# Kernel tuning notes

Hardware: AMD Instinct MI355X
Metric: run time of the kernel (lower is better)

Reference implementation:

```python
import jax, jax.numpy as jnp
import numpy as np
from jax import lax

B, C, H, W = 16, 128, 128, 128
COUT, KH, KW, K, RED, TEMP = 128, 3, 3, 4, 4, 30.0
ATTN_CH = max(C // RED, 1)

def setup_inputs() -> dict:
    key = jax.random.key(0)
    ks = jax.random.split(key, 7)
    fan_out = COUT * KH * KW
    std = np.sqrt(2.0 / fan_out)  # kaiming_normal fan_out, relu
    return {
        "x": jax.random.normal(ks[0], (B, C, H, W), dtype=jnp.float32),
        "weight": jax.random.normal(ks[1], (K, COUT, C, KH, KW), dtype=jnp.float32) * std,
        "bias": jnp.zeros((K, COUT), dtype=jnp.float32),
        "aw1": jax.random.normal(ks[2], (ATTN_CH, C), dtype=jnp.float32) * (1.0 / np.sqrt(C)),
        "ab1": jnp.zeros((ATTN_CH,), dtype=jnp.float32),
        "aw2": jax.random.normal(ks[3], (K, ATTN_CH), dtype=jnp.float32) * (1.0 / np.sqrt(ATTN_CH)),
        "ab2": jnp.zeros((K,), dtype=jnp.float32),
    }

def reference(x, weight, bias, aw1, ab1, aw2, ab2):
    # Attention branch: global avg pool -> 1x1 conv -> relu -> 1x1 conv
    pooled = jnp.mean(x, axis=(2, 3))                       # (B, C)
    h = jax.nn.relu(pooled @ aw1.T + ab1)                   # (B, attn_ch)
    scores = h @ aw2.T + ab2                                # (B, K)
    attn = jax.nn.softmax(scores / TEMP, axis=1)            # (B, K)

    # Per-sample aggregated kernel and bias
    agg_w = jnp.einsum('bk,koipq->boipq', attn, weight)     # (B, Cout, Cin, kH, kW)
    agg_b = attn @ bias                                     # (B, Cout)

    # Per-sample conv2d (stride 1, padding 1, dilation 1, groups 1)
    def conv_one(xi, wi):
        return lax.conv_general_dilated(
            xi[None], wi,
            window_strides=(1, 1),
            padding=((1, 1), (1, 1)),
            dimension_numbers=('NCHW', 'OIHW', 'NCHW'),
        )[0]

    out = jax.vmap(conv_one)(x, agg_w)                      # (B, Cout, H, W)
    return out + agg_b[:, :, None, None]
```

## Files before the change

kernel.cpp:

```cpp
#include <hip/hip_runtime.h>

typedef float f32x4 __attribute__((ext_vector_type(4)));
typedef short bf16x8 __attribute__((ext_vector_type(8)));

__device__ __forceinline__ unsigned short f2bf(float f) {
  unsigned u = __builtin_bit_cast(unsigned, f);
  u = (u + 0x7FFFu + ((u >> 16) & 1u)) >> 16;
  return (unsigned short)u;
}

__device__ __forceinline__ void async16(const unsigned short* g, unsigned short* l) {
  __builtin_amdgcn_global_load_lds(
      (__attribute__((address_space(1))) void*)g,
      (__attribute__((address_space(3))) void*)l, 16, 0, 0);
}

#define XT_ROW 16640

__global__ __launch_bounds__(256) void k_transpose(const float* __restrict__ x,
                                                   unsigned short* __restrict__ xt,
                                                   float* __restrict__ rowsum) {
  __shared__ unsigned short tile[128][128];
  __shared__ float psum[128][8];
  const int y = blockIdx.x, b = blockIdx.y;
  const int t = threadIdx.x;
  const int colb = (t & 7) * 16;
  const int cp = t >> 3;
  const int swz = (t & 7) << 3;
  for (int ci = 0; ci < 4; ++ci) {
    const int c = ci * 32 + cp;
    const int c2 = c ^ swz;
    const float* src = x + (((size_t)(b * 128 + c) * 128 + y) * 128 + colb);
    float s = 0.f;
#pragma unroll
    for (int j = 0; j < 16; j += 4) {
      float4 v = *(const float4*)(src + j);
      s += v.x + v.y + v.z + v.w;
      tile[colb + j + 0][c2] = f2bf(v.x);
      tile[colb + j + 1][c2] = f2bf(v.y);
      tile[colb + j + 2][c2] = f2bf(v.z);
      tile[colb + j + 3][c2] = f2bf(v.w);
    }
    psum[c][t & 7] = s;
  }
  __syncthreads();
#pragma unroll
  for (int it = 0; it < 8; ++it) {
    const int slot = t + it * 256;
    const int col = slot >> 4;
    const int cg = (slot & 15) * 8;
    const int c2 = cg ^ (((col >> 4) & 7) << 3);
    uint4 vv = *(const uint4*)&tile[col][c2];
    *(uint4*)(xt + (((size_t)b * 130 + y + 1) * 130 + col + 1) * 128 + cg) = vv;
  }
  if (t < 128) {
    float r = 0.f;
#pragma unroll
    for (int j = 0; j < 8; ++j) r += psum[t][j];
    rowsum[((size_t)b * 128 + t) * 128 + y] = r;
  }
}

__global__ __launch_bounds__(256) void k_border(unsigned short* __restrict__ xt) {
  const int b = blockIdx.y;
  const int idx = blockIdx.x * 256 + threadIdx.x;
  if (idx >= 8256) return;
  int row, col, ck;
  if (idx < 4160) {
    row = (idx < 2080) ? 0 : 129;
    const int s = idx % 2080;
    col = s >> 4;
    ck = s & 15;
  } else {
    const int s = idx - 4160;
    row = (s >> 5) + 1;
    col = (s & 16) ? 129 : 0;
    ck = s & 15;
  }
  uint4 z = {0, 0, 0, 0};
  *(uint4*)(xt + ((size_t)b * 130 + row) * 130 * 128 + (size_t)col * 128 + ck * 8) = z;
}

__global__ __launch_bounds__(128) void k_attn(const float* __restrict__ rowsum,
                                              const float* __restrict__ aw1,
                                              const float* __restrict__ ab1,
                                              const float* __restrict__ aw2,
                                              const float* __restrict__ ab2,
                                              const float* __restrict__ bias,
                                              float* __restrict__ attn,
                                              float* __restrict__ aggb) {
  __shared__ float pooled[128];
  __shared__ float h[32];
  __shared__ float at[4];
  const int b = blockIdx.x, t = threadIdx.x;
  const float* rs = rowsum + (size_t)(b * 128 + t) * 128;
  float s = 0.f;
  for (int yy = 0; yy < 128; ++yy) s += rs[yy];
  pooled[t] = s * (1.f / 16384.f);
  __syncthreads();
  if (t < 32) {
    float hv = ab1[t];
    for (int c = 0; c < 128; ++c) hv += pooled[c] * aw1[t * 128 + c];
    h[t] = fmaxf(hv, 0.f);
  }
  __syncthreads();
  if (t < 4) {
    float sc = ab2[t];
    for (int a = 0; a < 32; ++a) sc += h[a] * aw2[t * 32 + a];
    at[t] = sc * (1.f / 30.f);
  }
  __syncthreads();
  if (t == 0) {
    float m = fmaxf(fmaxf(at[0], at[1]), fmaxf(at[2], at[3]));
    float e0 = __expf(at[0] - m), e1 = __expf(at[1] - m);
    float e2 = __expf(at[2] - m), e3 = __expf(at[3] - m);
    float inv = 1.f / (e0 + e1 + e2 + e3);
    at[0] = e0 * inv; at[1] = e1 * inv; at[2] = e2 * inv; at[3] = e3 * inv;
  }
  __syncthreads();
  if (t < 4) attn[b * 4 + t] = at[t];
  float ab = 0.f;
  for (int k = 0; k < 4; ++k) ab += at[k] * bias[k * 128 + t];
  aggb[b * 128 + t] = ab;
}

__global__ __launch_bounds__(256) void k_aggw(const float* __restrict__ weight,
                                              const float* __restrict__ attn,
                                              unsigned short* __restrict__ aggw) {
  const int fid = blockIdx.x * 256 + threadIdx.x;
  const int kk = fid & 63;
  const int o = (fid >> 6) & 127;
  const int rest = fid >> 13;
  const int s = rest % 18;
  const int b = rest / 18;
  const int c = ((s & 1) << 6) + kk;
  const int pq = s >> 1;
  const size_t src = (size_t)o * 1152 + (size_t)c * 9 + pq;
  float v = attn[b * 4 + 0] * weight[src]
          + attn[b * 4 + 1] * weight[src + 147456]
          + attn[b * 4 + 2] * weight[src + 2 * 147456]
          + attn[b * 4 + 3] * weight[src + 3 * 147456];
  aggw[fid] = f2bf(v);
}

__global__ __launch_bounds__(512, 1) void k_conv(const unsigned short* __restrict__ xt,
                                                 const unsigned short* __restrict__ aggw,
                                                 const float* __restrict__ aggb,
                                                 float* __restrict__ out) {
  __shared__ unsigned short lds[73728];
  const int id = blockIdx.x;
  const int swz = (id & 7) * 128 + (id >> 3);
  const int b = swz >> 6;
  const int Y = (swz & 63) * 2;
  const int t = threadIdx.x;
  const int lane = t & 63, w = t >> 6;
  const int mw = w >> 2, nw = w & 3;
  const int l15 = lane & 15, lk = lane >> 4;
  const int e7 = l15 & 7;
  const int sl0 = (lk ^ e7) * 8;
  const int sl1 = ((4 ^ lk) ^ e7) * 8;
  const int baseA0 = (mw * 64 + l15) * 64 + sl0;
  const int baseA1 = (mw * 64 + l15) * 64 + sl1;
  const int baseB0 = 8192 + (nw * 64 + l15) * 64 + sl0;
  const int baseB1 = 8192 + (nw * 64 + l15) * 64 + sl1;

  const unsigned short* aS[2];
#pragma unroll
  for (int i = 0; i < 2; ++i) {
    const int c = i * 512 + t, o = c >> 3, k8 = c & 7;
    aS[i] = aggw + (size_t)b * 147456 + o * 64 + ((k8 ^ (o & 7)) * 8);
  }
  const unsigned short* bS[4];
#pragma unroll
  for (int i = 0; i < 4; ++i) {
    const int c = i * 512 + t, n = c >> 3, k8 = c & 7;
    const int r = n >> 7, col = n & 127;
    bS[i] = xt + ((size_t)(b * 130 + Y + r) * 130 + col) * 128 + ((k8 ^ (n & 7)) * 8);
  }

#define STA(jw, s2, i) async16(aS[i] + (s2) * 8192,                            \
                               &lds[(jw) * 24576 + ((i) * 512 + w * 64) * 8])
#define STB(jw, i, p2, q2, c02) async16(bS[i] + (p2) * XT_ROW + (q2) * 128 + (c02), \
                               &lds[(jw) * 24576 + 8192 + ((i) * 512 + w * 64) * 8])

  STA(0, 0, 0); STA(0, 0, 1);
  STB(0, 0, 0, 0, 0); STB(0, 1, 0, 0, 0); STB(0, 2, 0, 0, 0); STB(0, 3, 0, 0, 0);
  STA(1, 1, 0); STA(1, 1, 1);
  STB(1, 0, 0, 0, 64); STB(1, 1, 0, 0, 64); STB(1, 2, 0, 0, 64); STB(1, 3, 0, 0, 64);

  f32x4 acc[4][4] = {};

#pragma unroll
  for (int s = 0; s < 18; ++s) {
    const int jb = (s % 3) * 24576;
    const int s2 = s + 2, jw = s2 % 3;
    const int tap2 = s2 >> 1;
    const int p2 = tap2 / 3, q2 = tap2 - 3 * p2, c02 = (s2 & 1) << 6;
    const bool st = (s2 < 18);

    if (s < 17) { asm volatile("s_waitcnt vmcnt(6)" ::: "memory"); }
    else        { asm volatile("s_waitcnt vmcnt(0)" ::: "memory"); }
    __builtin_amdgcn_sched_barrier(0);
    __builtin_amdgcn_s_barrier();
    __builtin_amdgcn_sched_barrier(0);

    bf16x8 a0, a1, a2, a3, b0, b1, b2, b3;
    b0 = *(const bf16x8*)(&lds[jb + baseB0 + 0 * 1024]);
    b1 = *(const bf16x8*)(&lds[jb + baseB0 + 1 * 1024]);
    b2 = *(const bf16x8*)(&lds[jb + baseB0 + 2 * 1024]);
    b3 = *(const bf16x8*)(&lds[jb + baseB0 + 3 * 1024]);
    a0 = *(const bf16x8*)(&lds[jb + baseA0 + 0 * 1024]);
    a1 = *(const bf16x8*)(&lds[jb + baseA0 + 1 * 1024]);
    if (st) { STA(jw, s2, 0); STA(jw, s2, 1); }
    __builtin_amdgcn_s_barrier();
    __builtin_amdgcn_s_setprio(1);
    acc[0][0] = __builtin_amdgcn_mfma_f32_16x16x32_bf16(a0, b0, acc[0][0], 0, 0, 0);
    acc[0][1] = __builtin_amdgcn_mfma_f32_16x16x32_bf16(a0, b1, acc[0][1], 0, 0, 0);
    acc[0][2] = __builtin_amdgcn_mfma_f32_16x16x32_bf16(a0, b2, acc[0][2], 0, 0, 0);
    acc[0][3] = __builtin_amdgcn_mfma_f32_16x16x32_bf16(a0, b3, acc[0][3], 0, 0, 0);
    acc[1][0] = __builtin_amdgcn_mfma_f32_16x16x32_bf16(a1, b0, acc[1][0], 0, 0, 0);
    acc[1][1] = __builtin_amdgcn_mfma_f32_16x16x32_bf16(a1, b1, acc[1][1], 0, 0, 0);
    acc[1][2] = __builtin_amdgcn_mfma_f32_16x16x32_bf16(a1, b2, acc[1][2], 0, 0, 0);
    acc[1][3] = __builtin_amdgcn_mfma_f32_16x16x32_bf16(a1, b3, acc[1][3], 0, 0, 0);
    __builtin_amdgcn_s_setprio(0);
    __builtin_amdgcn_s_barrier();
    a2 = *(const bf16x8*)(&lds[jb + baseA0 + 2 * 1024]);
    a3 = *(const bf16x8*)(&lds[jb + baseA0 + 3 * 1024]);
    if (st) { STB(jw, 0, p2, q2, c02); STB(jw, 1, p2, q2, c02); }
    __builtin_amdgcn_s_barrier();
    __builtin_amdgcn_s_setprio(1);
    acc[2][0] = __builtin_amdgcn_mfma_f32_16x16x32_bf16(a2, b0, acc[2][0], 0, 0, 0);
    acc[2][1] = __builtin_amdgcn_mfma_f32_16x16x32_bf16(a2, b1, acc[2][1], 0, 0, 0);
    acc[2][2] = __builtin_amdgcn_mfma_f32_16x16x32_bf16(a2, b2, acc[2][2], 0, 0, 0);
    acc[2][3] = __builtin_amdgcn_mfma_f32_16x16x32_bf16(a2, b3, acc[2][3], 0, 0, 0);
    acc[3][0] = __builtin_amdgcn_mfma_f32_16x16x32_bf16(a3, b0, acc[3][0], 0, 0, 0);
    acc[3][1] = __builtin_amdgcn_mfma_f32_16x16x32_bf16(a3, b1, acc[3][1], 0, 0, 0);
    acc[3][2] = __builtin_amdgcn_mfma_f32_16x16x32_bf16(a3, b2, acc[3][2], 0, 0, 0);
    acc[3][3] = __builtin_amdgcn_mfma_f32_16x16x32_bf16(a3, b3, acc[3][3], 0, 0, 0);
    __builtin_amdgcn_s_setprio(0);
    __builtin_amdgcn_s_barrier();
    b0 = *(const bf16x8*)(&lds[jb + baseB1 + 0 * 1024]);
    b1 = *(const bf16x8*)(&lds[jb + baseB1 + 1 * 1024]);
    b2 = *(const bf16x8*)(&lds[jb + baseB1 + 2 * 1024]);
    b3 = *(const bf16x8*)(&lds[jb + baseB1 + 3 * 1024]);
    a0 = *(const bf16x8*)(&lds[jb + baseA1 + 0 * 1024]);
    a1 = *(const bf16x8*)(&lds[jb + baseA1 + 1 * 1024]);
    if (st) { STB(jw, 2, p2, q2, c02); STB(jw, 3, p2, q2, c02); }
    __builtin_amdgcn_s_barrier();
    __builtin_amdgcn_s_setprio(1);
    acc[0][0] = __builtin_amdgcn_mfma_f32_16x16x32_bf16(a0, b0, acc[0][0], 0, 0, 0);
    acc[0][1] = __builtin_amdgcn_mfma_f32_16x16x32_bf16(a0, b1, acc[0][1], 0, 0, 0);
    acc[0][2] = __builtin_amdgcn_mfma_f32_16x16x32_bf16(a0, b2, acc[0][2], 0, 0, 0);
    acc[0][3] = __builtin_amdgcn_mfma_f32_16x16x32_bf16(a0, b3, acc[0][3], 0, 0, 0);
    acc[1][0] = __builtin_amdgcn_mfma_f32_16x16x32_bf16(a1, b0, acc[1][0], 0, 0, 0);
    acc[1][1] = __builtin_amdgcn_mfma_f32_16x16x32_bf16(a1, b1, acc[1][1], 0, 0, 0);
    acc[1][2] = __builtin_amdgcn_mfma_f32_16x16x32_bf16(a1, b2, acc[1][2], 0, 0, 0);
    acc[1][3] = __builtin_amdgcn_mfma_f32_16x16x32_bf16(a1, b3, acc[1][3], 0, 0, 0);
    __builtin_amdgcn_s_setprio(0);
    __builtin_amdgcn_s_barrier();
    a2 = *(const bf16x8*)(&lds[jb + baseA1 + 2 * 1024]);
    a3 = *(const bf16x8*)(&lds[jb + baseA1 + 3 * 1024]);
    __builtin_amdgcn_s_barrier();
    __builtin_amdgcn_s_setprio(1);
    acc[2][0] = __builtin_amdgcn_mfma_f32_16x16x32_bf16(a2, b0, acc[2][0], 0, 0, 0);
    acc[2][1] = __builtin_amdgcn_mfma_f32_16x16x32_bf16(a2, b1, acc[2][1], 0, 0, 0);
    acc[2][2] = __builtin_amdgcn_mfma_f32_16x16x32_bf16(a2, b2, acc[2][2], 0, 0, 0);
    acc[2][3] = __builtin_amdgcn_mfma_f32_16x16x32_bf16(a2, b3, acc[2][3], 0, 0, 0);
    acc[3][0] = __builtin_amdgcn_mfma_f32_16x16x32_bf16(a3, b0, acc[3][0], 0, 0, 0);
    acc[3][1] = __builtin_amdgcn_mfma_f32_16x16x32_bf16(a3, b1, acc[3][1], 0, 0, 0);
    acc[3][2] = __builtin_amdgcn_mfma_f32_16x16x32_bf16(a3, b2, acc[3][2], 0, 0, 0);
    acc[3][3] = __builtin_amdgcn_mfma_f32_16x16x32_bf16(a3, b3, acc[3][3], 0, 0, 0);
    __builtin_amdgcn_s_setprio(0);
  }
#undef STA
#undef STB

  const int y = Y + (nw >> 1);
  const int colb = (nw & 1) * 64 + l15;
#pragma unroll
  for (int mi = 0; mi < 4; ++mi) {
    const int o = mw * 64 + mi * 16 + lk * 4;
#pragma unroll
    for (int rr = 0; rr < 4; ++rr) {
      const float bsv = aggb[b * 128 + o + rr];
      float* orow = out + ((size_t)(b * 128 + o + rr) * 128 + y) * 128 + colb;
      orow[0]  = acc[mi][0][rr] + bsv;
      orow[16] = acc[mi][1][rr] + bsv;
      orow[32] = acc[mi][2][rr] + bsv;
      orow[48] = acc[mi][3][rr] + bsv;
    }
  }
}

extern "C" void kernel_launch(void* const* d_in, const int* in_sizes, int n_in,
                              void* d_out, int out_size, void* d_ws, size_t ws_size,
                              hipStream_t stream) {
  const float* x      = (const float*)d_in[0];
  const float* weight = (const float*)d_in[1];
  const float* bias   = (const float*)d_in[2];
  const float* aw1    = (const float*)d_in[3];
  const float* ab1    = (const float*)d_in[4];
  const float* aw2    = (const float*)d_in[5];
  const float* ab2    = (const float*)d_in[6];
  float* out = (float*)d_out;

  char* ws = (char*)d_ws;
  unsigned short* xt   = (unsigned short*)ws;
  unsigned short* aggw = (unsigned short*)(ws + 69222400);
  float* rowsum        = (float*)(ws + 69222400 + 4718592);
  float* attn          = (float*)(ws + 69222400 + 4718592 + 1048576);
  float* aggb          = (float*)(ws + 69222400 + 4718592 + 1048576 + 256);

  hipLaunchKernelGGL(k_border, dim3(33, 16), dim3(256), 0, stream, xt);
  hipLaunchKernelGGL(k_transpose, dim3(128, 16), dim3(256), 0, stream, x, xt, rowsum);
  hipLaunchKernelGGL(k_attn, dim3(16), dim3(128), 0, stream,
                     rowsum, aw1, ab1, aw2, ab2, bias, attn, aggb);
  hipLaunchKernelGGL(k_aggw, dim3(9216), dim3(256), 0, stream, weight, attn, aggw);
  hipLaunchKernelGGL(k_conv, dim3(1024), dim3(512), 0, stream, xt, aggw, aggb, out);
}
```

Measured before the change: 157.8 us.

## Enlarge conv tile to four rows per block with double-buffered LDS

The conv kernel now computes a full 128-output-channel by 4-row (512-pixel) tile per block, with each wave owning all 128 output channels and 64 pixels. The grid is halved and each weight chunk is reused across twice as many pixels. The three-stage LDS ring with prefetch distance two is replaced by a two-buffer scheme with a full vmcnt(0) wait each step, and launch bounds now ask for two blocks per CU. Accumulators per thread double, raising register pressure, and the shallower prefetch may expose load latency.

```diff
diff --git a/kernel.cpp b/kernel.cpp
--- a/kernel.cpp
+++ b/kernel.cpp
@@ -143,26 +143,26 @@
   aggw[fid] = f2bf(v);
 }
 
-__global__ __launch_bounds__(512, 1) void k_conv(const unsigned short* __restrict__ xt,
+__global__ __launch_bounds__(512, 2) void k_conv(const unsigned short* __restrict__ xt,
                                                  const unsigned short* __restrict__ aggw,
                                                  const float* __restrict__ aggb,
                                                  float* __restrict__ out) {
-  __shared__ unsigned short lds[73728];
+  __shared__ unsigned short lds[81920];
   const int id = blockIdx.x;
-  const int swz = (id & 7) * 128 + (id >> 3);
-  const int b = swz >> 6;
-  const int Y = (swz & 63) * 2;
+  const int swz = (id & 7) * 64 + (id >> 3);
+  const int b = swz >> 5;
+  const int Y = (swz & 31) * 4;
   const int t = threadIdx.x;
-  const int lane = t & 63, w = t >> 6;
-  const int mw = w >> 2, nw = w & 3;
+  const int lane = t & 63, nw = t >> 6;
   const int l15 = lane & 15, lk = lane >> 4;
   const int e7 = l15 & 7;
   const int sl0 = (lk ^ e7) * 8;
   const int sl1 = ((4 ^ lk) ^ e7) * 8;
-  const int baseA0 = (mw * 64 + l15) * 64 + sl0;
-  const int baseA1 = (mw * 64 + l15) * 64 + sl1;
-  const int baseB0 = 8192 + (nw * 64 + l15) * 64 + sl0;
-  const int baseB1 = 8192 + (nw * 64 + l15) * 64 + sl1;
+  const int baseA0 = l15 * 64 + sl0;
+  const int baseA1 = l15 * 64 + sl1;
+  const int nrow = (nw >> 1) * 128 + (nw & 1) * 64 + l15;
+  const int baseB0 = 8192 + nrow * 64 + sl0;
+  const int baseB1 = 8192 + nrow * 64 + sl1;
 
   const unsigned short* aS[2];
 #pragma unroll
@@ -170,36 +170,37 @@
     const int c = i * 512 + t, o = c >> 3, k8 = c & 7;
     aS[i] = aggw + (size_t)b * 147456 + o * 64 + ((k8 ^ (o & 7)) * 8);
   }
-  const unsigned short* bS[4];
-#pragma unroll
-  for (int i = 0; i < 4; ++i) {
+  const unsigned short* bS[8];
+#pragma unroll
+  for (int i = 0; i < 8; ++i) {
     const int c = i * 512 + t, n = c >> 3, k8 = c & 7;
     const int r = n >> 7, col = n & 127;
-    bS[i] = xt + ((size_t)(b * 130 + Y + r) * 130 + col) * 128 + ((k8 ^ (n & 7)) * 8);
-  }
-
-#define STA(jw, s2, i) async16(aS[i] + (s2) * 8192,                            \
-                               &lds[(jw) * 24576 + ((i) * 512 + w * 64) * 8])
-#define STB(jw, i, p2, q2, c02) async16(bS[i] + (p2) * XT_ROW + (q2) * 128 + (c02), \
-                               &lds[(jw) * 24576 + 8192 + ((i) * 512 + w * 64) * 8])
+    bS[i] = xt + ((size_t)(b * 130 + Y + r) * 130 + col) * 128 + ((k8 ^ (col & 7)) * 8);
+  }
+
+  const int wu = (t >> 6) * 64;
+#define STA(jb, sv, i) async16(aS[i] + (size_t)(sv) * 8192,                    \
+                               &lds[(jb) + ((i) * 512 + wu) * 8])
+#define STB(jb, pqv, i) async16(bS[i] + (pqv),                                 \
+                               &lds[(jb) + 8192 + ((i) * 512 + wu) * 8])
 
   STA(0, 0, 0); STA(0, 0, 1);
-  STB(0, 0, 0, 0, 0); STB(0, 1, 0, 0, 0); STB(0, 2, 0, 0, 0); STB(0, 3, 0, 0, 0);
-  STA(1, 1, 0); STA(1, 1, 1);
-  STB(1, 0, 0, 0, 64); STB(1, 1, 0, 0, 64); STB(1, 2, 0, 0, 64); STB(1, 3, 0, 0, 64);
-
-  f32x4 acc[4][4] = {};
+#pragma unroll
+  for (int i = 0; i < 8; ++i) STB(0, 0, i);
+
+  f32x4 acc[8][4] = {};
 
 #pragma unroll
   for (int s = 0; s < 18; ++s) {
-    const int jb = (s % 3) * 24576;
-    const int s2 = s + 2, jw = s2 % 3;
-    const int tap2 = s2 >> 1;
-    const int p2 = tap2 / 3, q2 = tap2 - 3 * p2, c02 = (s2 & 1) << 6;
-    const bool st = (s2 < 18);
-
-    if (s < 17) { asm volatile("s_waitcnt vmcnt(6)" ::: "memory"); }
-    else        { asm volatile("s_waitcnt vmcnt(0)" ::: "memory"); }
+    const int jb = (s & 1) * 40960;
+    const int jn = ((s + 1) & 1) * 40960;
+    const int s1 = s + 1;
+    const int tap1 = s1 >> 1;
+    const int p1 = tap1 / 3, q1 = tap1 - 3 * p1;
+    const int pq1 = (p1 * 130 + q1) * 128 + ((s1 & 1) << 6);
+    const bool st = (s1 < 18);
+
+    asm volatile("s_waitcnt vmcnt(0)" ::: "memory");
     __builtin_amdgcn_sched_barrier(0);
     __builtin_amdgcn_s_barrier();
     __builtin_amdgcn_sched_barrier(0);
@@ -211,32 +212,40 @@
     b3 = *(const bf16x8*)(&lds[jb + baseB0 + 3 * 1024]);
     a0 = *(const bf16x8*)(&lds[jb + baseA0 + 0 * 1024]);
     a1 = *(const bf16x8*)(&lds[jb + baseA0 + 1 * 1024]);
-    if (st) { STA(jw, s2, 0); STA(jw, s2, 1); }
-    __builtin_amdgcn_s_barrier();
-    __builtin_amdgcn_s_setprio(1);
-    acc[0][0] = __builtin_amdgcn_mfma_f32_16x16x32_bf16(a0, b0, acc[0][0], 0, 0, 0);
-    acc[0][1] = __builtin_amdgcn_mfma_f32_16x16x32_bf16(a0, b1, acc[0][1], 0, 0, 0);
-    acc[0][2] = __builtin_amdgcn_mfma_f32_16x16x32_bf16(a0, b2, acc[0][2], 0, 0, 0);
-    acc[0][3] = __builtin_amdgcn_mfma_f32_16x16x32_bf16(a0, b3, acc[0][3], 0, 0, 0);
-    acc[1][0] = __builtin_amdgcn_mfma_f32_16x16x32_bf16(a1, b0, acc[1][0], 0, 0, 0);
-    acc[1][1] = __builtin_amdgcn_mfma_f32_16x16x32_bf16(a1, b1, acc[1][1], 0, 0, 0);
-    acc[1][2] = __builtin_amdgcn_mfma_f32_16x16x32_bf16(a1, b2, acc[1][2], 0, 0, 0);
-    acc[1][3] = __builtin_amdgcn_mfma_f32_16x16x32_bf16(a1, b3, acc[1][3], 0, 0, 0);
-    __builtin_amdgcn_s_setprio(0);
-    __builtin_amdgcn_s_barrier();
     a2 = *(const bf16x8*)(&lds[jb + baseA0 + 2 * 1024]);
     a3 = *(const bf16x8*)(&lds[jb + baseA0 + 3 * 1024]);
-    if (st) { STB(jw, 0, p2, q2, c02); STB(jw, 1, p2, q2, c02); }
-    __builtin_amdgcn_s_barrier();
+    if (st) { STA(jn, s1, 0); STA(jn, s1, 1); STB(jn, pq1, 0); STB(jn, pq1, 1); }
+    __builtin_amdgcn_sched_barrier(0);
+    __builtin_amdgcn_s_barrier();
+    __builtin_amdgcn_sched_barrier(0);
     __builtin_amdgcn_s_setprio(1);
-    acc[2][0] = __builtin_amdgcn_mfma_f32_16x16x32_bf16(a2, b0, acc[2][0], 0, 0, 0);
-    acc[2][1] = __builtin_amdgcn_mfma_f32_16x16x32_bf16(a2, b1, acc[2][1], 0, 0, 0);
-    acc[2][2] = __builtin_amdgcn_mfma_f32_16x16x32_bf16(a2, b2, acc[2][2], 0, 0, 0);
-    acc[2][3] = __builtin_amdgcn_mfma_f32_16x16x32_bf16(a2, b3, acc[2][3], 0, 0, 0);
-    acc[3][0] = __builtin_amdgcn_mfma_f32_16x16x32_bf16(a3, b0, acc[3][0], 0, 0, 0);
-    acc[3][1] = __builtin_amdgcn_mfma_f32_16x16x32_bf16(a3, b1, acc[3][1], 0, 0, 0);
-    acc[3][2] = __builtin_amdgcn_mfma_f32_16x16x32_bf16(a3, b2, acc[3][2], 0, 0, 0);
-    acc[3][3] = __builtin_amdgcn_mfma_f32_16x16x32_bf16(a3, b3, acc[3][3], 0, 0, 0);
+#pragma unroll
+    for (int ni = 0; ni < 4; ++ni) {
+      const bf16x8 bb = (ni == 0) ? b0 : (ni == 1) ? b1 : (ni == 2) ? b2 : b3;
+      acc[0][ni] = __builtin_amdgcn_mfma_f32_16x16x32_bf16(a0, bb, acc[0][ni], 0, 0, 0);
+      acc[1][ni] = __builtin_amdgcn_mfma_f32_16x16x32_bf16(a1, bb, acc[1][ni], 0, 0, 0);
+      acc[2][ni] = __builtin_amdgcn_mfma_f32_16x16x32_bf16(a2, bb, acc[2][ni], 0, 0, 0);
+      acc[3][ni] = __builtin_amdgcn_mfma_f32_16x16x32_bf16(a3, bb, acc[3][ni], 0, 0, 0);
+    }
+    __builtin_amdgcn_s_setprio(0);
+    __builtin_amdgcn_s_barrier();
+    a0 = *(const bf16x8*)(&lds[jb + baseA0 + 4 * 1024]);
+    a1 = *(const bf16x8*)(&lds[jb + baseA0 + 5 * 1024]);
+    a2 = *(const bf16x8*)(&lds[jb + baseA0 + 6 * 1024]);
+    a3 = *(const bf16x8*)(&lds[jb + baseA0 + 7 * 1024]);
+    if (st) { STB(jn, pq1, 2); STB(jn, pq1, 3); }
+    __builtin_amdgcn_sched_barrier(0);
+    __builtin_amdgcn_s_barrier();
+    __builtin_amdgcn_sched_barrier(0);
+    __builtin_amdgcn_s_setprio(1);
+#pragma unroll
+    for (int ni = 0; ni < 4; ++ni) {
+      const bf16x8 bb = (ni == 0) ? b0 : (ni == 1) ? b1 : (ni == 2) ? b2 : b3;
+      acc[4][ni] = __builtin_amdgcn_mfma_f32_16x16x32_bf16(a0, bb, acc[4][ni], 0, 0, 0);
+      acc[5][ni] = __builtin_amdgcn_mfma_f32_16x16x32_bf16(a1, bb, acc[5][ni], 0, 0, 0);
+      acc[6][ni] = __builtin_amdgcn_mfma_f32_16x16x32_bf16(a2, bb, acc[6][ni], 0, 0, 0);
+      acc[7][ni] = __builtin_amdgcn_mfma_f32_16x16x32_bf16(a3, bb, acc[7][ni], 0, 0, 0);
+    }
     __builtin_amdgcn_s_setprio(0);
     __builtin_amdgcn_s_barrier();
     b0 = *(const bf16x8*)(&lds[jb + baseB1 + 0 * 1024]);
@@ -245,31 +254,40 @@
     b3 = *(const bf16x8*)(&lds[jb + baseB1 + 3 * 1024]);
     a0 = *(const bf16x8*)(&lds[jb + baseA1 + 0 * 1024]);
     a1 = *(const bf16x8*)(&lds[jb + baseA1 + 1 * 1024]);
-    if (st) { STB(jw, 2, p2, q2, c02); STB(jw, 3, p2, q2, c02); }
-    __builtin_amdgcn_s_barrier();
-    __builtin_amdgcn_s_setprio(1);
-    acc[0][0] = __builtin_amdgcn_mfma_f32_16x16x32_bf16(a0, b0, acc[0][0], 0, 0, 0);
-    acc[0][1] = __builtin_amdgcn_mfma_f32_16x16x32_bf16(a0, b1, acc[0][1], 0, 0, 0);
-    acc[0][2] = __builtin_amdgcn_mfma_f32_16x16x32_bf16(a0, b2, acc[0][2], 0, 0, 0);
-    acc[0][3] = __builtin_amdgcn_mfma_f32_16x16x32_bf16(a0, b3, acc[0][3], 0, 0, 0);
-    acc[1][0] = __builtin_amdgcn_mfma_f32_16x16x32_bf16(a1, b0, acc[1][0], 0, 0, 0);
-    acc[1][1] = __builtin_amdgcn_mfma_f32_16x16x32_bf16(a1, b1, acc[1][1], 0, 0, 0);
-    acc[1][2] = __builtin_amdgcn_mfma_f32_16x16x32_bf16(a1, b2, acc[1][2], 0, 0, 0);
-    acc[1][3] = __builtin_amdgcn_mfma_f32_16x16x32_bf16(a1, b3, acc[1][3], 0, 0, 0);
-    __builtin_amdgcn_s_setprio(0);
-    __builtin_amdgcn_s_barrier();
     a2 = *(const bf16x8*)(&lds[jb + baseA1 + 2 * 1024]);
     a3 = *(const bf16x8*)(&lds[jb + baseA1 + 3 * 1024]);
-    __builtin_amdgcn_s_barrier();
+    if (st) { STB(jn, pq1, 4); STB(jn, pq1, 5); }
+    __builtin_amdgcn_sched_barrier(0);
+    __builtin_amdgcn_s_barrier();
+    __builtin_amdgcn_sched_barrier(0);
     __builtin_amdgcn_s_setprio(1);
-    acc[2][0] = __builtin_amdgcn_mfma_f32_16x16x32_bf16(a2, b0, acc[2][0], 0, 0, 0);
-    acc[2][1] = __builtin_amdgcn_mfma_f32_16x16x32_bf16(a2, b1, acc[2][1], 0, 0, 0);
-    acc[2][2] = __builtin_amdgcn_mfma_f32_16x16x32_bf16(a2, b2, acc[2][2], 0, 0, 0);
-    acc[2][3] = __builtin_amdgcn_mfma_f32_16x16x32_bf16(a2, b3, acc[2][3], 0, 0, 0);
-    acc[3][0] = __builtin_amdgcn_mfma_f32_16x16x32_bf16(a3, b0, acc[3][0], 0, 0, 0);
-    acc[3][1] = __builtin_amdgcn_mfma_f32_16x16x32_bf16(a3, b1, acc[3][1], 0, 0, 0);
-    acc[3][2] = __builtin_amdgcn_mfma_f32_16x16x32_bf16(a3, b2, acc[3][2], 0, 0, 0);
-    acc[3][3] = __builtin_amdgcn_mfma_f32_16x16x32_bf16(a3, b3, acc[3][3], 0, 0, 0);
+#pragma unroll
+    for (int ni = 0; ni < 4; ++ni) {
+      const bf16x8 bb = (ni == 0) ? b0 : (ni == 1) ? b1 : (ni == 2) ? b2 : b3;
+      acc[0][ni] = __builtin_amdgcn_mfma_f32_16x16x32_bf16(a0, bb, acc[0][ni], 0, 0, 0);
+      acc[1][ni] = __builtin_amdgcn_mfma_f32_16x16x32_bf16(a1, bb, acc[1][ni], 0, 0, 0);
+      acc[2][ni] = __builtin_amdgcn_mfma_f32_16x16x32_bf16(a2, bb, acc[2][ni], 0, 0, 0);
+      acc[3][ni] = __builtin_amdgcn_mfma_f32_16x16x32_bf16(a3, bb, acc[3][ni], 0, 0, 0);
+    }
+    __builtin_amdgcn_s_setprio(0);
+    __builtin_amdgcn_s_barrier();
+    a0 = *(const bf16x8*)(&lds[jb + baseA1 + 4 * 1024]);
+    a1 = *(const bf16x8*)(&lds[jb + baseA1 + 5 * 1024]);
+    a2 = *(const bf16x8*)(&lds[jb + baseA1 + 6 * 1024]);
+    a3 = *(const bf16x8*)(&lds[jb + baseA1 + 7 * 1024]);
+    if (st) { STB(jn, pq1, 6); STB(jn, pq1, 7); }
+    __builtin_amdgcn_sched_barrier(0);
+    __builtin_amdgcn_s_barrier();
+    __builtin_amdgcn_sched_barrier(0);
+    __builtin_amdgcn_s_setprio(1);
+#pragma unroll
+    for (int ni = 0; ni < 4; ++ni) {
+      const bf16x8 bb = (ni == 0) ? b0 : (ni == 1) ? b1 : (ni == 2) ? b2 : b3;
+      acc[4][ni] = __builtin_amdgcn_mfma_f32_16x16x32_bf16(a0, bb, acc[4][ni], 0, 0, 0);
+      acc[5][ni] = __builtin_amdgcn_mfma_f32_16x16x32_bf16(a1, bb, acc[5][ni], 0, 0, 0);
+      acc[6][ni] = __builtin_amdgcn_mfma_f32_16x16x32_bf16(a2, bb, acc[6][ni], 0, 0, 0);
+      acc[7][ni] = __builtin_amdgcn_mfma_f32_16x16x32_bf16(a3, bb, acc[7][ni], 0, 0, 0);
+    }
     __builtin_amdgcn_s_setprio(0);
   }
 #undef STA
@@ -278,8 +296,8 @@
   const int y = Y + (nw >> 1);
   const int colb = (nw & 1) * 64 + l15;
 #pragma unroll
-  for (int mi = 0; mi < 4; ++mi) {
-    const int o = mw * 64 + mi * 16 + lk * 4;
+  for (int mi = 0; mi < 8; ++mi) {
+    const int o = mi * 16 + lk * 4;
 #pragma unroll
     for (int rr = 0; rr < 4; ++rr) {
       const float bsv = aggb[b * 128 + o + rr];
@@ -316,5 +334,5 @@
   hipLaunchKernelGGL(k_attn, dim3(16), dim3(128), 0, stream,
                      rowsum, aw1, ab1, aw2, ab2, bias, attn, aggb);
   hipLaunchKernelGGL(k_aggw, dim3(9216), dim3(256), 0, stream, weight, attn, aggw);
-  hipLaunchKernelGGL(k_conv, dim3(1024), dim3(512), 0, stream, xt, aggw, aggb, out);
-}
+  hipLaunchKernelGGL(k_conv, dim3(512), dim3(512), 0, stream, xt, aggw, aggb, out);
+}
```

Measured after the change: 155.0 us. Within noise of the previous version (-1.8%).
